# Kernel optimization log

Measured on AMD Instinct MI355X. Metric: run time of the kernel, lower is better.

The kernel has to match this reference:

```python
import jax, jax.numpy as jnp
import numpy as np

NUM_HEADS = 16
HEAD_DIM = 32  # dim=512 / num_heads=16


def _rel_pos_bias(table, index, window_area):
    # table: [(2W-1)^2, H], index: [N, N] int -> bias [1, H, N, N]
    bias = table[index.reshape(-1)].reshape(window_area, window_area, -1)
    return jnp.transpose(bias, (2, 0, 1))[None]


def setup_inputs() -> dict:
    key = jax.random.key(0)
    ks = jax.random.split(key, 6)
    B, N, C = 256, 196, 512
    x = jax.random.normal(ks[0], (B, N, C), dtype=jnp.float32)
    qkv_w = jax.random.normal(ks[1], (3 * C, C), dtype=jnp.float32) * 0.02
    proj_w = jax.random.normal(ks[2], (C, C), dtype=jnp.float32) * 0.02
    proj_b = jax.random.normal(ks[3], (C,), dtype=jnp.float32) * 0.02
    rel_pos_bias_table = jax.random.normal(ks[4], (729, NUM_HEADS), dtype=jnp.float32) * 0.02
    rel_pos_index = jax.random.randint(ks[5], (N, N), 0, 729, dtype=jnp.int64)
    return {
        "x": x,
        "qkv_w": qkv_w,
        "proj_w": proj_w,
        "proj_b": proj_b,
        "rel_pos_bias_table": rel_pos_bias_table,
        "rel_pos_index": rel_pos_index,
        "window_area": N,
    }


def reference(x, qkv_w, proj_w, proj_b, rel_pos_bias_table, rel_pos_index, window_area):
    B, N, C = x.shape
    H, hd = NUM_HEADS, HEAD_DIM
    scale = hd ** -0.5
    # qkv projection (no bias), split into q,k,v: [B, H, N, hd]
    qkv = (x @ qkv_w.T).reshape(B, N, 3, H, hd)
    qkv = jnp.transpose(qkv, (2, 0, 3, 1, 4))
    q, k, v = qkv[0], qkv[1], qkv[2]
    attn = jnp.einsum("bhnd,bhmd->bhnm", q * scale, k)
    attn = attn + _rel_pos_bias(rel_pos_bias_table, rel_pos_index, window_area)
    attn = jax.nn.softmax(attn, axis=-1)
    out = jnp.einsum("bhnm,bhmd->bhnd", attn, v)
    out = jnp.transpose(out, (0, 2, 1, 3)).reshape(B, N, C)
    return out @ proj_w.T + proj_b
```

## Files before the change

kernel.cpp:

```cpp
#include <hip/hip_runtime.h>
#include <hip/hip_bf16.h>


typedef unsigned short u16;
typedef unsigned int u32;
typedef __attribute__((ext_vector_type(8))) short bf16x8;
typedef __attribute__((ext_vector_type(4))) float f32x4;

#define AS1 __attribute__((address_space(1)))
#define AS3 __attribute__((address_space(3)))

__device__ __forceinline__ u16 f2bf(float f) {
  union { float f; unsigned u; } c; c.f = f;
  unsigned r = ((c.u >> 16) & 1u) + 0x7fffu;
  return (u16)((c.u + r) >> 16);
}

__global__ __launch_bounds__(256) void cvt_f32_bf16(const float* __restrict__ in,
                                                    u16* __restrict__ out, int n) {
  int i = (blockIdx.x * 256 + threadIdx.x) * 4;
  if (i >= n) return;
  float4 v = *(const float4*)(in + i);
  ushort4 o;
  o.x = f2bf(v.x); o.y = f2bf(v.y); o.z = f2bf(v.z); o.w = f2bf(v.w);
  *(ushort4*)(out + i) = o;
}

__global__ __launch_bounds__(256) void zero_vt_pad(u16* __restrict__ vt) {
  int i = blockIdx.x * 256 + threadIdx.x;
  if (i >= 4096 * 32 * 36) return;
  int row = i / 36, c = i - row * 36;
  vt[row * 232 + 196 + c] = 0;
}

__global__ __launch_bounds__(256) void build_bias(const float* __restrict__ table,
                                                  const int* __restrict__ idx,
                                                  u16* __restrict__ outb) {
  int e = blockIdx.x * 256 + threadIdx.x;
  int r = e & 3, lane = (e >> 2) & 63, rest = e >> 8;
  int mt = rest % 14; rest /= 14;
  int nt = rest % 13; int h = rest / 13;
  int n = nt * 16 + (lane & 15);
  int m = mt * 16 + ((lane >> 4) << 2) + r;
  float v;
  if (m < 196) {
    int nc = n < 196 ? n : 195;
    v = table[idx[nc * 196 + m] * 16 + h];
  } else {
    v = -1e30f;
  }
  outb[e] = f2bf(v);
}

template<int KT>
__device__ __forceinline__ void ktile(u16* __restrict__ SMEM,
    const u16* __restrict__ gA0, const u16* __restrict__ gA1,
    const u16* __restrict__ gB0, const u16* __restrict__ gB1,
    int wbase, int rdA, int rdB, f32x4 (&acc)[8][4]) {
  constexpr int BUF = KT & 1, OBUF = BUF ^ 1;
  constexpr bool S01 = (KT < 7);
  constexpr bool S23 = (KT < 6);
  constexpr int C1 = (KT + 1) * 64;
  constexpr int C2 = (KT + 2) * 64;
  bf16x8 afr[4], bfr[4];

#define LOADPAIR(dst, g0, g1, coloff)                                          \
  __builtin_amdgcn_global_load_lds((const AS1 void*)((g0) + (coloff)),         \
      (AS3 void*)&SMEM[(dst) + wbase], 16, 0, 0);                              \
  __builtin_amdgcn_global_load_lds((const AS1 void*)((g1) + (coloff)),         \
      (AS3 void*)&SMEM[(dst) + 4096 + wbase], 16, 0, 0);
#define MFMA16(FH)                                                             \
  __builtin_amdgcn_s_setprio(1);                                               \
  _Pragma("unroll") for (int q = 0; q < 4; ++q)                                \
    _Pragma("unroll") for (int j = 0; j < 4; ++j)                              \
      acc[(FH)*4 + q][j] = __builtin_amdgcn_mfma_f32_16x16x32_bf16(            \
          afr[q], bfr[j], acc[(FH)*4 + q][j], 0, 0, 0);                        \
  __builtin_amdgcn_s_setprio(0);

#pragma unroll
  for (int j = 0; j < 4; ++j) bfr[j] = *(const bf16x8*)&SMEM[rdB + BUF * 16384 + j * 512];
#pragma unroll
  for (int q = 0; q < 4; ++q) afr[q] = *(const bf16x8*)&SMEM[rdA + BUF * 16384 + q * 512];
  if constexpr (S01) { LOADPAIR(OBUF * 16384 + 8192, gA0, gA1, C1 + 32) }
  __builtin_amdgcn_s_barrier();
  asm volatile("s_waitcnt lgkmcnt(0)" ::: "memory");
  MFMA16(0)
  __builtin_amdgcn_s_barrier();
#pragma unroll
  for (int q = 0; q < 4; ++q) afr[q] = *(const bf16x8*)&SMEM[rdA + BUF * 16384 + (q + 4) * 512];
  if constexpr (S01) { LOADPAIR(32768 + OBUF * 16384 + 8192, gB0, gB1, C1 + 32) }
  __builtin_amdgcn_s_barrier();
  asm volatile("s_waitcnt lgkmcnt(0)" ::: "memory");
  MFMA16(1)
  if constexpr (KT < 7) { asm volatile("s_waitcnt vmcnt(8)" ::: "memory"); }
  else                  { asm volatile("s_waitcnt vmcnt(0)" ::: "memory"); }
  __builtin_amdgcn_s_barrier();
#pragma unroll
  for (int j = 0; j < 4; ++j) bfr[j] = *(const bf16x8*)&SMEM[rdB + BUF * 16384 + 8192 + j * 512];
#pragma unroll
  for (int q = 0; q < 4; ++q) afr[q] = *(const bf16x8*)&SMEM[rdA + BUF * 16384 + 8192 + q * 512];
  if constexpr (S23) { LOADPAIR(BUF * 16384, gA0, gA1, C2) }
  __builtin_amdgcn_s_barrier();
  asm volatile("s_waitcnt lgkmcnt(0)" ::: "memory");
  MFMA16(0)
  __builtin_amdgcn_s_barrier();
#pragma unroll
  for (int q = 0; q < 4; ++q) afr[q] = *(const bf16x8*)&SMEM[rdA + BUF * 16384 + 8192 + (q + 4) * 512];
  if constexpr (S23) { LOADPAIR(32768 + BUF * 16384, gB0, gB1, C2) }
  __builtin_amdgcn_s_barrier();
  asm volatile("s_waitcnt lgkmcnt(0)" ::: "memory");
  MFMA16(1)
  if constexpr (KT < 6)       { asm volatile("s_waitcnt vmcnt(8)" ::: "memory"); }
  else if constexpr (KT == 6) { asm volatile("s_waitcnt vmcnt(4)" ::: "memory"); }
  __builtin_amdgcn_s_barrier();
#undef LOADPAIR
#undef MFMA16
}

template<int EPI>
__global__ __launch_bounds__(512, 2) void gemm8p(
    const u16* __restrict__ A, const u16* __restrict__ Bt,
    u16* __restrict__ q, u16* __restrict__ kk, u16* __restrict__ vt,
    const float* __restrict__ pbias, float* __restrict__ out) {
  constexpr int NWGX = (EPI == 0) ? 6 : 2;
  constexpr int NWG = NWGX * 196;
  __shared__ __align__(16) u16 SMEM[65536];

  int id = blockIdx.y * NWGX + blockIdx.x;
  int nf = (id & 7) * (NWG >> 3) + (id >> 3);
  const int bx = nf / NWGX, by = nf - (nf / NWGX) * NWGX;

  const int tid = threadIdx.x;
  const int w = tid >> 6, l = tid & 63;
  const int lr = l & 15, lg = l >> 4;
  const int wm = w >> 2, wn = w & 3;

  const int gsw = (l & 3) ^ ((l >> 3) & 3);
  const u16* gA0 = A + (size_t)(bx * 256 + w * 16 + (l >> 2)) * 512 + gsw * 8;
  const u16* gA1 = gA0 + 65536;
  const u16* gB0 = Bt + (size_t)(by * 256 + w * 16 + (l >> 2)) * 512 + gsw * 8;
  const u16* gB1 = gB0 + 65536;
  const int wbase = w * 512;

  const int rsw = (lg ^ ((lr >> 1) & 3)) * 8;
  const int rdA = (wm * 128 + lr) * 32 + rsw;
  const int rdB = 32768 + (wn * 64 + lr) * 32 + rsw;

  f32x4 acc[8][4] = {};

#define PLP(dst, g0, g1, coloff)                                               \
  __builtin_amdgcn_global_load_lds((const AS1 void*)((g0) + (coloff)),         \
      (AS3 void*)&SMEM[(dst) + wbase], 16, 0, 0);                              \
  __builtin_amdgcn_global_load_lds((const AS1 void*)((g1) + (coloff)),         \
      (AS3 void*)&SMEM[(dst) + 4096 + wbase], 16, 0, 0);
  PLP(0, gA0, gA1, 0)
  asm volatile("" ::: "memory");
  PLP(32768, gB0, gB1, 0)
  asm volatile("" ::: "memory");
  PLP(8192, gA0, gA1, 32)
  asm volatile("" ::: "memory");
  PLP(32768 + 8192, gB0, gB1, 32)
  asm volatile("" ::: "memory");
  PLP(16384, gA0, gA1, 64)
  asm volatile("" ::: "memory");
  PLP(32768 + 16384, gB0, gB1, 64)
#undef PLP
  asm volatile("s_waitcnt vmcnt(8)" ::: "memory");
  __builtin_amdgcn_s_barrier();

  ktile<0>(SMEM, gA0, gA1, gB0, gB1, wbase, rdA, rdB, acc);
  ktile<1>(SMEM, gA0, gA1, gB0, gB1, wbase, rdA, rdB, acc);
  ktile<2>(SMEM, gA0, gA1, gB0, gB1, wbase, rdA, rdB, acc);
  ktile<3>(SMEM, gA0, gA1, gB0, gB1, wbase, rdA, rdB, acc);
  ktile<4>(SMEM, gA0, gA1, gB0, gB1, wbase, rdA, rdB, acc);
  ktile<5>(SMEM, gA0, gA1, gB0, gB1, wbase, rdA, rdB, acc);
  ktile<6>(SMEM, gA0, gA1, gB0, gB1, wbase, rdA, rdB, acc);
  ktile<7>(SMEM, gA0, gA1, gB0, gB1, wbase, rdA, rdB, acc);

  if (EPI == 0) {
    const int t = by >> 1;
    const int colbase = by * 256;
    const float s = (t == 0) ? 0.17677669529663687f : 1.0f;
#pragma unroll
    for (int p = 0; p < 2; ++p) {
      __syncthreads();
      if (wm == p) {
        if (t < 2) {
#pragma unroll
        for (int f = 0; f < 8; ++f)
#pragma unroll
          for (int j2 = 0; j2 < 4; ++j2)
#pragma unroll
            for (int r = 0; r < 4; ++r)
              SMEM[(f * 16 + lg * 4 + r) * 264 + wn * 64 + j2 * 16 + lr] =
                  f2bf(acc[f][j2][r] * s);
        } else {
#pragma unroll
        for (int f = 0; f < 8; ++f)
#pragma unroll
          for (int j2 = 0; j2 < 4; ++j2)
#pragma unroll
            for (int r = 0; r < 4; ++r)
              SMEM[(wn * 64 + j2 * 16 + lr) * 136 + f * 16 + lg * 4 + r] =
                  f2bf(acc[f][j2][r]);
        }
      }
      __syncthreads();
      const int growbase = bx * 256 + p * 128;
      if (t < 2) {
        u16* dst = (t == 0) ? q : kk;
        const int lrow = tid >> 2, ch = tid & 3;
        const int grow = growbase + lrow;
        const int bb2 = grow / 196, nn = grow - bb2 * 196;
#pragma unroll
        for (int i = 0; i < 8; ++i) {
          const int colle = (ch + i * 4) * 8;
          bf16x8 vv = *(const bf16x8*)&SMEM[lrow * 264 + colle];
          const int col = colbase + colle;
          const int h = (col >> 5) & 15, dd = col & 31;
          *(bf16x8*)&dst[((size_t)(bb2 * 16 + h) * 196 + nn) * 32 + dd] = vv;
        }
      } else {
        const int cl = tid >> 1, half = tid & 1;
        const int col = colbase + cl;
        const int h = (col >> 5) & 15, dd = col & 31;
#pragma unroll
        for (int i = 0; i < 8; ++i) {
          const int r0 = growbase + half * 64 + i * 8;
          bf16x8 vv = *(const bf16x8*)&SMEM[cl * 136 + half * 64 + i * 8];
          const int bb2 = r0 / 196, nn = r0 - bb2 * 196;
          if (nn + 8 <= 196) {
            *(bf16x8*)&vt[((size_t)(bb2 * 16 + h) * 32 + dd) * 232 + nn] = vv;
          } else {
#pragma unroll
            for (int e = 0; e < 8; ++e) {
              const int rr = r0 + e;
              const int b3 = rr / 196, n3 = rr - b3 * 196;
              vt[((size_t)(b3 * 16 + h) * 32 + dd) * 232 + n3] = (u16)((short*)&vv)[e];
            }
          }
        }
      }
    }
  } else {
    const int colbase = by * 256 + wn * 64;
    const int rowb = bx * 256 + wm * 128 + lg * 4;
#pragma unroll
    for (int f = 0; f < 8; ++f) {
      const int row0 = rowb + f * 16;
#pragma unroll
      for (int j2 = 0; j2 < 4; ++j2) {
        const int col = colbase + j2 * 16 + lr;
        const float pb = pbias[col];
#pragma unroll
        for (int r = 0; r < 4; ++r)
          out[(size_t)(row0 + r) * 512 + col] = acc[f][j2][r] + pb;
      }
    }
  }
}

__global__ __launch_bounds__(256, 4) void attn_kernel(
    const u16* __restrict__ q, const u16* __restrict__ kk,
    const u16* __restrict__ vt, const u16* __restrict__ biasA,
    u16* __restrict__ ao) {
  __shared__ u16 Ks[196 * 40];
  __shared__ u16 Vs[32 * 232];
  const int bhd = blockIdx.x;
  const int h = bhd >> 8, bb = bhd & 255;
  const int bh = bb * 16 + h;
  const int tid = threadIdx.x, w = tid >> 6, l = tid & 63;
  const int lr = l & 15, lg = l >> 4;

  {
    const u16* kg = kk + (size_t)bh * (196 * 32);
#pragma unroll
    for (int p = 0; p < 4; ++p) {
      int m = p * 64 + (tid >> 2);
      if (m < 196) {
        int c = (tid & 3) * 8;
        *(bf16x8*)&Ks[m * 40 + c] = *(const bf16x8*)(kg + m * 32 + c);
      }
    }
    const u16* vg = vt + (size_t)bh * (32 * 232);
#pragma unroll
    for (int p = 0; p < 4; ++p) {
      int off = (p * 256 + tid) * 8;
      if (off < 32 * 232) *(bf16x8*)&Vs[off] = *(const bf16x8*)(vg + off);
    }
  }
  __syncthreads();

  const u16* biasH = biasA + (size_t)h * (13 * 14 * 256);
  const int sA = ((l & 16) << 1) + lr;
  const int sB = sA + 16;
  const bool hi = (l & 32) != 0;

  for (int nt = w; nt < 13; nt += 4) {
    int nq = nt * 16 + lr; if (nq > 195) nq = 195;
    bf16x8 qa = *(const bf16x8*)(q + ((size_t)bh * 196 + nq) * 32 + lg * 8);

    u32 pk[14][2];
    float ssum = 0.f;
#pragma unroll
    for (int mt = 0; mt < 14; ++mt) {
      int row = mt * 16 + lr; if (row > 195) row = 195;
      bf16x8 kb = *(const bf16x8*)&Ks[row * 40 + lg * 8];
      const ushort4 b4 = *(const ushort4*)(biasH + ((nt * 14 + mt) * 64 + l) * 4);
      f32x4 c;
      c[0] = __uint_as_float(((u32)b4.x) << 16);
      c[1] = __uint_as_float(((u32)b4.y) << 16);
      c[2] = __uint_as_float(((u32)b4.z) << 16);
      c[3] = __uint_as_float(((u32)b4.w) << 16);
      f32x4 S = __builtin_amdgcn_mfma_f32_16x16x32_bf16(kb, qa, c, 0, 0, 0);
      float e0 = __expf(S[0]), e1 = __expf(S[1]);
      float e2 = __expf(S[2]), e3 = __expf(S[3]);
      ssum += (e0 + e1) + (e2 + e3);
      asm("v_cvt_pk_bf16_f32 %0, %1, %2" : "=v"(pk[mt][0]) : "v"(e0), "v"(e1));
      asm("v_cvt_pk_bf16_f32 %0, %1, %2" : "=v"(pk[mt][1]) : "v"(e2), "v"(e3));
    }
    ssum += __shfl_xor(ssum, 16);
    ssum += __shfl_xor(ssum, 32);
    float invT = __builtin_amdgcn_rcpf(ssum);

    f32x4 O0 = {}, O1 = {};
#pragma unroll
    for (int ks = 0; ks < 7; ++ks) {
      u32 a0 = (u32)__shfl((int)pk[2 * ks][0], sA);
      u32 a1 = (u32)__shfl((int)pk[2 * ks][1], sA);
      u32 a2 = (u32)__shfl((int)pk[2 * ks][0], sB);
      u32 a3 = (u32)__shfl((int)pk[2 * ks][1], sB);
      u32 c0 = (u32)__shfl((int)pk[2 * ks + 1][0], sA);
      u32 c1 = (u32)__shfl((int)pk[2 * ks + 1][1], sA);
      u32 c2 = (u32)__shfl((int)pk[2 * ks + 1][0], sB);
      u32 c3 = (u32)__shfl((int)pk[2 * ks + 1][1], sB);
      bf16x8 pa;
      ((u32*)&pa)[0] = hi ? c0 : a0;
      ((u32*)&pa)[1] = hi ? c1 : a1;
      ((u32*)&pa)[2] = hi ? c2 : a2;
      ((u32*)&pa)[3] = hi ? c3 : a3;
      bf16x8 v0 = *(const bf16x8*)&Vs[lr * 232 + ks * 32 + lg * 8];
      bf16x8 v1 = *(const bf16x8*)&Vs[(16 + lr) * 232 + ks * 32 + lg * 8];
      O0 = __builtin_amdgcn_mfma_f32_16x16x32_bf16(pa, v0, O0, 0, 0, 0);
      O1 = __builtin_amdgcn_mfma_f32_16x16x32_bf16(pa, v1, O1, 0, 0, 0);
    }

    float inv[4];
#pragma unroll
    for (int r = 0; r < 4; ++r) inv[r] = __shfl(invT, lg * 4 + r);
    const int nr0 = nt * 16 + lg * 4;
#pragma unroll
    for (int r = 0; r < 4; ++r) {
      int nr = nr0 + r;
      if (nr < 196) {
        size_t base = ((size_t)bb * 196 + nr) * 512 + h * 32;
        ao[base + lr] = f2bf(O0[r] * inv[r]);
        ao[base + 16 + lr] = f2bf(O1[r] * inv[r]);
      }
    }
  }
}

extern "C" void kernel_launch(void* const* d_in, const int* in_sizes, int n_in,
                              void* d_out, int out_size, void* d_ws, size_t ws_size,
                              hipStream_t stream) {
  const float* x      = (const float*)d_in[0];
  const float* qkv_w  = (const float*)d_in[1];
  const float* proj_w = (const float*)d_in[2];
  const float* proj_b = (const float*)d_in[3];
  const float* table  = (const float*)d_in[4];
  const int*   ridx   = (const int*)d_in[5];
  float* out = (float*)d_out;

  char* ws = (char*)d_ws;
  u16*   xb    = (u16*)(ws);
  u16*   qwb   = (u16*)(ws + 51380224);
  u16*   pwb   = (u16*)(ws + 52953088);
  u16*   qb    = (u16*)(ws + 53477376);
  u16*   kb    = (u16*)(ws + 104857600);
  u16*   vtb   = (u16*)(ws + 156237824);
  u16*   biasA = (u16*)(ws + 217055232);

  cvt_f32_bf16<<<25088, 256, 0, stream>>>(x, xb, 25690112);
  cvt_f32_bf16<<<768, 256, 0, stream>>>(qkv_w, qwb, 786432);
  cvt_f32_bf16<<<256, 256, 0, stream>>>(proj_w, pwb, 262144);
  build_bias<<<2912, 256, 0, stream>>>(table, ridx, biasA);
  zero_vt_pad<<<18432, 256, 0, stream>>>(vtb);

  gemm8p<0><<<dim3(6, 196), 512, 0, stream>>>(xb, qwb, qb, kb, vtb, nullptr, nullptr);
  attn_kernel<<<4096, 256, 0, stream>>>(qb, kb, vtb, biasA, xb );
  gemm8p<1><<<dim3(2, 196), 512, 0, stream>>>(xb, pwb, nullptr, nullptr, nullptr, proj_b, out);
}
```

Before: 275.9 us.

## Write V row-major from QKV GEMM and transpose into LDS inside attention

The QKV GEMM epilogue now writes V in the same [b,h,n,d] layout as Q and K, removing the separate transposed-V store path and the zero_vt_pad kernel launch. The attention kernel instead loads V row-wise and scatters it transposed into shared memory with scalar LDS stores, zeroing the pad columns itself. The attention launch bound's occupancy hint is also lowered from 4 to 2 blocks per CU. This removes one kernel and the strided global stores, but adds scalar LDS writes, which may bank-conflict, and possibly lower occupancy in attention.

Measured after the change: 270.4 us. -2.0%, faster.

```diff
diff --git a/kernel.cpp b/kernel.cpp
--- a/kernel.cpp
+++ b/kernel.cpp
@@ -24,13 +24,6 @@
   ushort4 o;
   o.x = f2bf(v.x); o.y = f2bf(v.y); o.z = f2bf(v.z); o.w = f2bf(v.w);
   *(ushort4*)(out + i) = o;
-}
-
-__global__ __launch_bounds__(256) void zero_vt_pad(u16* __restrict__ vt) {
-  int i = blockIdx.x * 256 + threadIdx.x;
-  if (i >= 4096 * 32 * 36) return;
-  int row = i / 36, c = i - row * 36;
-  vt[row * 232 + 196 + c] = 0;
 }
 
 __global__ __launch_bounds__(256) void build_bias(const float* __restrict__ table,
@@ -120,7 +113,7 @@
 template<int EPI>
 __global__ __launch_bounds__(512, 2) void gemm8p(
     const u16* __restrict__ A, const u16* __restrict__ Bt,
-    u16* __restrict__ q, u16* __restrict__ kk, u16* __restrict__ vt,
+    u16* __restrict__ q, u16* __restrict__ kk, u16* __restrict__ vv,
     const float* __restrict__ pbias, float* __restrict__ out) {
   constexpr int NWGX = (EPI == 0) ? 6 : 2;
   constexpr int NWG = NWGX * 196;
@@ -179,13 +172,13 @@
 
   if (EPI == 0) {
     const int t = by >> 1;
+    u16* dst = (t == 0) ? q : (t == 1) ? kk : vv;
     const int colbase = by * 256;
     const float s = (t == 0) ? 0.17677669529663687f : 1.0f;
 #pragma unroll
     for (int p = 0; p < 2; ++p) {
       __syncthreads();
       if (wm == p) {
-        if (t < 2) {
 #pragma unroll
         for (int f = 0; f < 8; ++f)
 #pragma unroll
@@ -194,52 +187,19 @@
             for (int r = 0; r < 4; ++r)
               SMEM[(f * 16 + lg * 4 + r) * 264 + wn * 64 + j2 * 16 + lr] =
                   f2bf(acc[f][j2][r] * s);
-        } else {
-#pragma unroll
-        for (int f = 0; f < 8; ++f)
-#pragma unroll
-          for (int j2 = 0; j2 < 4; ++j2)
-#pragma unroll
-            for (int r = 0; r < 4; ++r)
-              SMEM[(wn * 64 + j2 * 16 + lr) * 136 + f * 16 + lg * 4 + r] =
-                  f2bf(acc[f][j2][r]);
-        }
       }
       __syncthreads();
       const int growbase = bx * 256 + p * 128;
-      if (t < 2) {
-        u16* dst = (t == 0) ? q : kk;
-        const int lrow = tid >> 2, ch = tid & 3;
-        const int grow = growbase + lrow;
-        const int bb2 = grow / 196, nn = grow - bb2 * 196;
-#pragma unroll
-        for (int i = 0; i < 8; ++i) {
-          const int colle = (ch + i * 4) * 8;
-          bf16x8 vv = *(const bf16x8*)&SMEM[lrow * 264 + colle];
-          const int col = colbase + colle;
-          const int h = (col >> 5) & 15, dd = col & 31;
-          *(bf16x8*)&dst[((size_t)(bb2 * 16 + h) * 196 + nn) * 32 + dd] = vv;
-        }
-      } else {
-        const int cl = tid >> 1, half = tid & 1;
-        const int col = colbase + cl;
+      const int lrow = tid >> 2, ch = tid & 3;
+      const int grow = growbase + lrow;
+      const int bb2 = grow / 196, nn = grow - bb2 * 196;
+#pragma unroll
+      for (int i = 0; i < 8; ++i) {
+        const int colle = (ch + i * 4) * 8;
+        bf16x8 vvx = *(const bf16x8*)&SMEM[lrow * 264 + colle];
+        const int col = colbase + colle;
         const int h = (col >> 5) & 15, dd = col & 31;
-#pragma unroll
-        for (int i = 0; i < 8; ++i) {
-          const int r0 = growbase + half * 64 + i * 8;
-          bf16x8 vv = *(const bf16x8*)&SMEM[cl * 136 + half * 64 + i * 8];
-          const int bb2 = r0 / 196, nn = r0 - bb2 * 196;
-          if (nn + 8 <= 196) {
-            *(bf16x8*)&vt[((size_t)(bb2 * 16 + h) * 32 + dd) * 232 + nn] = vv;
-          } else {
-#pragma unroll
-            for (int e = 0; e < 8; ++e) {
-              const int rr = r0 + e;
-              const int b3 = rr / 196, n3 = rr - b3 * 196;
-              vt[((size_t)(b3 * 16 + h) * 32 + dd) * 232 + n3] = (u16)((short*)&vv)[e];
-            }
-          }
-        }
+        *(bf16x8*)&dst[((size_t)(bb2 * 16 + h) * 196 + nn) * 32 + dd] = vvx;
       }
     }
   } else {
@@ -260,9 +220,9 @@
   }
 }
 
-__global__ __launch_bounds__(256, 4) void attn_kernel(
+__global__ __launch_bounds__(256, 2) void attn_kernel(
     const u16* __restrict__ q, const u16* __restrict__ kk,
-    const u16* __restrict__ vt, const u16* __restrict__ biasA,
+    const u16* __restrict__ vv, const u16* __restrict__ biasA,
     u16* __restrict__ ao) {
   __shared__ u16 Ks[196 * 40];
   __shared__ u16 Vs[32 * 232];
@@ -274,19 +234,22 @@
 
   {
     const u16* kg = kk + (size_t)bh * (196 * 32);
+    const u16* vg = vv + (size_t)bh * (196 * 32);
+    for (int k = tid; k < 32 * 36; k += 256) {
+      int d = k / 36, c = k - d * 36;
+      Vs[d * 232 + 196 + c] = 0;
+    }
 #pragma unroll
     for (int p = 0; p < 4; ++p) {
       int m = p * 64 + (tid >> 2);
       if (m < 196) {
-        int c = (tid & 3) * 8;
-        *(bf16x8*)&Ks[m * 40 + c] = *(const bf16x8*)(kg + m * 32 + c);
-      }
-    }
-    const u16* vg = vt + (size_t)bh * (32 * 232);
-#pragma unroll
-    for (int p = 0; p < 4; ++p) {
-      int off = (p * 256 + tid) * 8;
-      if (off < 32 * 232) *(bf16x8*)&Vs[off] = *(const bf16x8*)(vg + off);
+        int c8 = (tid & 3) * 8;
+        *(bf16x8*)&Ks[m * 40 + c8] = *(const bf16x8*)(kg + m * 32 + c8);
+        bf16x8 v8 = *(const bf16x8*)(vg + m * 32 + c8);
+#pragma unroll
+        for (int e = 0; e < 8; ++e)
+          Vs[(c8 + e) * 232 + m] = (u16)((short*)&v8)[e];
+      }
     }
   }
   __syncthreads();
@@ -378,16 +341,15 @@
   u16*   pwb   = (u16*)(ws + 52953088);
   u16*   qb    = (u16*)(ws + 53477376);
   u16*   kb    = (u16*)(ws + 104857600);
-  u16*   vtb   = (u16*)(ws + 156237824);
+  u16*   vb    = (u16*)(ws + 156237824);
   u16*   biasA = (u16*)(ws + 217055232);
 
   cvt_f32_bf16<<<25088, 256, 0, stream>>>(x, xb, 25690112);
   cvt_f32_bf16<<<768, 256, 0, stream>>>(qkv_w, qwb, 786432);
   cvt_f32_bf16<<<256, 256, 0, stream>>>(proj_w, pwb, 262144);
   build_bias<<<2912, 256, 0, stream>>>(table, ridx, biasA);
-  zero_vt_pad<<<18432, 256, 0, stream>>>(vtb);
-
-  gemm8p<0><<<dim3(6, 196), 512, 0, stream>>>(xb, qwb, qb, kb, vtb, nullptr, nullptr);
-  attn_kernel<<<4096, 256, 0, stream>>>(qb, kb, vtb, biasA, xb );
+
+  gemm8p<0><<<dim3(6, 196), 512, 0, stream>>>(xb, qwb, qb, kb, vb, nullptr, nullptr);
+  attn_kernel<<<4096, 256, 0, stream>>>(qb, kb, vb, biasA, xb );
   gemm8p<1><<<dim3(2, 196), 512, 0, stream>>>(xb, pwb, nullptr, nullptr, nullptr, proj_b, out);
 }
```
